# Kernel tuning notes

Hardware: AMD Instinct MI355X
Metric: run time of the kernel (lower is better)

The kernel has to match this reference:

```python
import jax, jax.numpy as jnp
import numpy as np

N_NODES = 100000
NEG_SLOPE = 0.2


def glorot(key, shape):
    fan_in, fan_out = shape[0], shape[-1]
    lim = jnp.sqrt(6.0 / (fan_in + fan_out))
    return jax.random.uniform(key, shape, jnp.float32, -lim, lim)


def setup_inputs() -> dict:
    key = jax.random.key(0)
    ks = jax.random.split(key, 16)
    x = jax.random.normal(ks[0], (N_NODES, 128), jnp.float32)
    edge_index = jax.random.randint(ks[1], (2, 1600000), 0, N_NODES, jnp.int64)
    H1, C1 = 4, 32
    C2 = 64
    return {
        "x": x,
        "edge_index": edge_index,
        # layer 1: GATv2Conv(128 -> 32, heads=4, concat)
        "Wl1": glorot(ks[2], (128, H1 * C1)), "bl1": jnp.zeros((H1 * C1,), jnp.float32),
        "Wr1": glorot(ks[3], (128, H1 * C1)), "br1": jnp.zeros((H1 * C1,), jnp.float32),
        "att1": glorot(ks[4], (H1, C1)),
        "bias1": jnp.zeros((H1 * C1,), jnp.float32),
        # layer 2: GATv2Conv(128 -> 64, heads=1, concat)
        "Wl2": glorot(ks[5], (H1 * C1, C2)), "bl2": jnp.zeros((C2,), jnp.float32),
        "Wr2": glorot(ks[6], (H1 * C1, C2)), "br2": jnp.zeros((C2,), jnp.float32),
        "att2": glorot(ks[7], (1, C2)),
        "bias2": jnp.zeros((C2,), jnp.float32),
    }


def gatv2_layer(x, src, dst, Wl, bl, Wr, br, att, bias):
    # x: [N, F_in]; src/dst: [E] (self-loops already appended)
    H, C = att.shape
    n = x.shape[0]
    xl = (x @ Wl + bl).reshape(n, H, C)  # source transform
    xr = (x @ Wr + br).reshape(n, H, C)  # target transform
    e = jax.nn.leaky_relu(xl[src] + xr[dst], NEG_SLOPE)          # [E, H, C]
    score = jnp.einsum('ehc,hc->eh', e, att)                     # [E, H]
    # segment softmax over incoming edges of each destination node
    smax = jax.ops.segment_max(score, dst, num_segments=n)       # [N, H]
    ex = jnp.exp(score - smax[dst])
    denom = jax.ops.segment_sum(ex, dst, num_segments=n)
    alpha = ex / denom[dst]                                      # [E, H]
    out = jax.ops.segment_sum(alpha[:, :, None] * xl[src], dst, num_segments=n)
    return out.reshape(n, H * C) + bias


def reference(x, edge_index, Wl1, bl1, Wr1, br1, att1, bias1,
              Wl2, bl2, Wr2, br2, att2, bias2):
    n = x.shape[0]
    loops = jnp.arange(n, dtype=edge_index.dtype)
    src = jnp.concatenate([edge_index[0], loops])
    dst = jnp.concatenate([edge_index[1], loops])
    h = gatv2_layer(x, src, dst, Wl1, bl1, Wr1, br1, att1, bias1)
    h = jax.nn.relu(h)
    out = gatv2_layer(h, src, dst, Wl2, bl2, Wr2, br2, att2, bias2)
    return out
```

## Files before the change

kernel.cpp:

```cpp
#include <hip/hip_runtime.h>
#include <hip/hip_fp16.h>

#define NEG 0.2f

typedef _Float16 f16x8 __attribute__((ext_vector_type(8)));
typedef _Float16 f16x2 __attribute__((ext_vector_type(2)));
typedef float    f32x4 __attribute__((ext_vector_type(4)));

__device__ __forceinline__ float fdot2h(__half2 a, __half2 b, float c) {
    return __builtin_amdgcn_fdot2(__builtin_bit_cast(f16x2, a),
                                  __builtin_bit_cast(f16x2, b), c, false);
}

__device__ __forceinline__ __half2 u2h2(unsigned int u) {
    return __builtin_bit_cast(__half2, u);
}

__device__ __forceinline__ __half2 hmax2(__half2 a, __half2 b) {
    unsigned int ua = __builtin_bit_cast(unsigned int, a);
    unsigned int ub = __builtin_bit_cast(unsigned int, b);
    unsigned int ud;
    asm("v_pk_max_f16 %0, %1, %2" : "=v"(ud) : "v"(ua), "v"(ub));
    return __builtin_bit_cast(__half2, ud);
}

template<int CTRL>
__device__ __forceinline__ float dppadd(float x) {
    int xi = __builtin_bit_cast(int, x);
    int yi = __builtin_amdgcn_update_dpp(0, xi, CTRL, 0xf, 0xf, true);
    return x + __builtin_bit_cast(float, yi);
}

template<int COLS, bool IN_F16, bool HPL>
__global__ __launch_bounds__(256) void xform_k(
    const float* __restrict__ Xf, const __half* __restrict__ Xh,
    const float* __restrict__ Wl, const float* __restrict__ bl,
    const float* __restrict__ Wr, const float* __restrict__ br,
    __half* __restrict__ YL, __half* __restrict__ YR, int nrows)
{
    constexpr int CPW = COLS / 2;
    __shared__ _Float16 Ws[COLS * 136];

    const int t = threadIdx.x;
    for (int i = t; i < 128 * COLS; i += 256) {
        int k = i / COLS, c = i % COLS;
        const float* Wp = (c >= CPW) ? Wr : Wl;
        int lc = c - ((c >= CPW) ? CPW : 0);
        Ws[c * 136 + k] = (_Float16)Wp[(long)k * CPW + lc];
    }
    __syncthreads();

    const int lane = t & 63, wv = t >> 6;
    const int m = lane & 15, quad = lane >> 4;

    float bv[COLS / 16];
    #pragma unroll
    for (int ct = 0; ct < COLS / 16; ++ct) {
        int col = ct * 16 + m;
        bv[ct] = (col >= CPW) ? br[col - CPW] : bl[col];
    }

    const int ntiles = (nrows + 15) >> 4;
    const int stride = gridDim.x * 4;

    int tile = blockIdx.x * 4 + wv;
    if (tile >= ntiles) return;

    f16x8 A0[4], A1[4];

    auto loadA = [&](int tl, f16x8* Af) {
        int row = tl * 16 + m;
        if (row >= nrows) row = nrows - 1;
        if constexpr (IN_F16) {
            const uint4* Xp = (const uint4*)(Xh + (long)row * 128);
            #pragma unroll
            for (int ks = 0; ks < 4; ++ks) {
                uint4 v = Xp[ks * 4 + quad];
                Af[ks] = __builtin_bit_cast(f16x8, v);
            }
        } else {
            const float4* Xp = (const float4*)(Xf + (long)row * 128);
            #pragma unroll
            for (int ks = 0; ks < 4; ++ks) {
                float4 a = Xp[ks * 8 + quad * 2];
                float4 b = Xp[ks * 8 + quad * 2 + 1];
                _Float16 h[8] = {(_Float16)a.x,(_Float16)a.y,(_Float16)a.z,(_Float16)a.w,
                                 (_Float16)b.x,(_Float16)b.y,(_Float16)b.z,(_Float16)b.w};
                Af[ks] = *(f16x8*)h;
            }
        }
    };

    loadA(tile, A0);

    for (; tile < ntiles; tile += stride) {
        int nt = tile + stride;
        if (nt < ntiles) loadA(nt, A1);

        const int row0 = tile * 16;
        #pragma unroll
        for (int ct = 0; ct < COLS / 16; ++ct) {
            f32x4 acc = (f32x4){0.f, 0.f, 0.f, 0.f};
            #pragma unroll
            for (int ks = 0; ks < 4; ++ks) {
                f16x8 Bf = *(const f16x8*)&Ws[(ct * 16 + m) * 136 + ks * 32 + quad * 8];
                acc = __builtin_amdgcn_mfma_f32_16x16x32_f16(A0[ks], Bf, acc, 0, 0, 0);
            }
            int col = ct * 16 + m;
            int which = col >= CPW;
            int lc = col - (which ? CPW : 0);
            _Float16* Y = (_Float16*)(which ? YR : YL);
            int rb = row0 + quad * 4;
            #pragma unroll
            for (int g = 0; g < 4; ++g) {
                int r = rb + g;
                if (r < nrows) {
                    long idx;
                    if (HPL && !which)
                        idx = (long)(lc >> 6) * ((long)nrows * 64) + (long)r * 64 + (lc & 63);
                    else
                        idx = (long)r * CPW + lc;
                    Y[idx] = (_Float16)(acc[g] + bv[ct]);
                }
            }
        }
        #pragma unroll
        for (int ks = 0; ks < 4; ++ks) A0[ks] = A1[ks];
    }
}

__global__ __launch_bounds__(256) void h1_k(
    const int* __restrict__ ei, int* __restrict__ gh, int E0, int ET, int NBK)
{
    __shared__ int h[256];
    const int t = threadIdx.x, blk = blockIdx.x;
    h[t] = 0;
    __syncthreads();
    int e = blk * 4096 + t;
    #pragma unroll
    for (int u = 0; u < 16; ++u, e += 256) {
        if (e < ET) {
            int dst = (e < E0) ? ei[E0 + e] : (e - E0);
            atomicAdd(&h[dst >> 9], 1);
        }
    }
    __syncthreads();
    gh[t * NBK + blk] = h[t];
}

__global__ __launch_bounds__(256) void scan1_k(
    const int* __restrict__ cnt, int* __restrict__ loc, int* __restrict__ bsum, int n)
{
    __shared__ int wsum[4];
    int t = threadIdx.x;
    int i0 = blockIdx.x * 1024 + t * 4;
    int4 v;
    v.x = (i0 + 0 < n) ? cnt[i0 + 0] : 0;
    v.y = (i0 + 1 < n) ? cnt[i0 + 1] : 0;
    v.z = (i0 + 2 < n) ? cnt[i0 + 2] : 0;
    v.w = (i0 + 3 < n) ? cnt[i0 + 3] : 0;
    int tsum = v.x + v.y + v.z + v.w;
    int incl = tsum;
    #pragma unroll
    for (int s = 1; s < 64; s <<= 1) {
        int u = __shfl_up(incl, s, 64);
        if ((t & 63) >= s) incl += u;
    }
    int wid = t >> 6;
    if ((t & 63) == 63) wsum[wid] = incl;
    __syncthreads();
    int woff = 0;
    #pragma unroll
    for (int w = 0; w < 4; ++w) if (w < wid) woff += wsum[w];
    int ex = woff + incl - tsum;
    if (i0 + 0 < n) loc[i0 + 0] = ex;
    if (i0 + 1 < n) loc[i0 + 1] = ex + v.x;
    if (i0 + 2 < n) loc[i0 + 2] = ex + v.x + v.y;
    if (i0 + 3 < n) loc[i0 + 3] = ex + v.x + v.y + v.z;
    if (t == 255) bsum[blockIdx.x] = woff + incl;
}

__global__ void scan2_k(const int* __restrict__ bsum, int* __restrict__ bcarry,
                        int M, int* __restrict__ total_out)
{
    int lane = threadIdx.x;
    int carry = 0;
    for (int base = 0; base < M; base += 64) {
        int i = base + lane;
        int v = (i < M) ? bsum[i] : 0;
        int incl = v;
        #pragma unroll
        for (int s = 1; s < 64; s <<= 1) {
            int u = __shfl_up(incl, s, 64);
            if (lane >= s) incl += u;
        }
        if (i < M) bcarry[i] = carry + incl - v;
        carry += __shfl(incl, 63, 64);
    }
    if (lane == 0) *total_out = carry;
}

__global__ __launch_bounds__(256) void scan3_k(
    int* __restrict__ off, const int* __restrict__ bcarry, int n)
{
    int i = blockIdx.x * 256 + threadIdx.x;
    if (i >= n) return;
    off[i] += bcarry[i >> 10];
}

__global__ __launch_bounds__(256) void sc1_k(
    const int* __restrict__ ei, const int* __restrict__ gh,
    uint2* __restrict__ rec, int E0, int ET, int NBK)
{
    __shared__ int lofs[256];
    const int t = threadIdx.x, blk = blockIdx.x;
    lofs[t] = gh[t * NBK + blk];
    __syncthreads();
    int e = blk * 4096 + t;
    #pragma unroll
    for (int u = 0; u < 16; ++u, e += 256) {
        if (e < ET) {
            int src = (e < E0) ? ei[e]      : (e - E0);
            int dst = (e < E0) ? ei[E0 + e] : (e - E0);
            int p = atomicAdd(&lofs[dst >> 9], 1);
            rec[p] = make_uint2((unsigned)src, (unsigned)dst);
        }
    }
}

__global__ __launch_bounds__(256) void p2_k(
    const uint2* __restrict__ rec, const int* __restrict__ gh,
    int* __restrict__ srcs, int* __restrict__ off, int N, int NBK)
{
    __shared__ int hist[512];
    __shared__ int sc[2][512];
    __shared__ int curo[512];
    const int t = threadIdx.x;
    const int b = blockIdx.x;
    const int base = gh[b * NBK];
    const int end  = gh[(b + 1) * NBK];
    hist[t] = 0; hist[t + 256] = 0;
    __syncthreads();
    for (int i = base + t; i < end; i += 256) {
        uint2 r = rec[i];
        atomicAdd(&hist[r.y & 511], 1);
    }
    __syncthreads();
    sc[0][t] = hist[t]; sc[0][t + 256] = hist[t + 256];
    __syncthreads();
    int pp = 0;
    for (int s = 1; s < 512; s <<= 1, pp ^= 1) {
        int j0 = t, j1 = t + 256;
        sc[pp ^ 1][j0] = sc[pp][j0] + ((j0 >= s) ? sc[pp][j0 - s] : 0);
        sc[pp ^ 1][j1] = sc[pp][j1] + ((j1 >= s) ? sc[pp][j1 - s] : 0);
        __syncthreads();
    }
    {
        int j0 = t, j1 = t + 256;
        int e0 = base + sc[pp][j0] - hist[j0];
        int e1 = base + sc[pp][j1] - hist[j1];
        curo[j0] = e0;
        curo[j1] = e1;
        int d0 = b * 512 + j0, d1 = b * 512 + j1;
        if (d0 < N) off[d0] = e0;
        if (d1 < N) off[d1] = e1;
    }
    __syncthreads();
    for (int i = base + t; i < end; i += 256) {
        uint2 r = rec[i];
        int pos = atomicAdd(&curo[r.y & 511], 1);
        srcs[pos] = (int)r.x;
    }
}

template<bool RELU>
__global__ __launch_bounds__(256) void fused128hp_k(
    const __half* __restrict__ XLp, const __half* __restrict__ XR,
    const float* __restrict__ ATT, const int* __restrict__ srcs,
    const int* __restrict__ off, const float* __restrict__ bias,
    __half* __restrict__ OUT, int N, int p)
{
    const int t   = threadIdx.x;
    const int d   = blockIdx.x * 32 + (t >> 3);
    const int sub = t & 7;
    const bool nv = d < N;

    int a = 0, b = 0;
    if (nv) { a = off[d]; b = off[d + 1]; }

    __half2 xr[4] = { u2h2(0), u2h2(0), u2h2(0), u2h2(0) };
    if (nv) {
        uint4 ur = *(const uint4*)(XR + (long)d * 128 + p * 64 + sub * 8);
        xr[0] = u2h2(ur.x); xr[1] = u2h2(ur.y); xr[2] = u2h2(ur.z); xr[3] = u2h2(ur.w);
    }
    float4 at0f = ((const float4*)ATT)[p * 16 + sub * 2];
    float4 at1f = ((const float4*)ATT)[p * 16 + sub * 2 + 1];
    __half2 at[4] = { __floats2half2_rn(at0f.x, at0f.y), __floats2half2_rn(at0f.z, at0f.w),
                      __floats2half2_rn(at1f.x, at1f.y), __floats2half2_rn(at1f.z, at1f.w) };
    const __half2 neg2 = __float2half2_rn(NEG);

    float l = 0.f;
    float accv[8] = {0.f,0.f,0.f,0.f,0.f,0.f,0.f,0.f};

    const uint4* XL4 = (const uint4*)(XLp + (size_t)p * N * 64);

    if (b > a) {
        const int bm1 = b - 1;
        int sA = srcs[a];
        uint4 r0 = XL4[(long)sA * 8 + sub];
        int i1 = (a + 1 < bm1) ? a + 1 : bm1;
        int sB = srcs[i1];
        uint4 r1 = XL4[(long)sB * 8 + sub];
        int i2 = (a + 2 < bm1) ? a + 2 : bm1;
        int s2 = srcs[i2];

        for (int e = a; e < b; ++e) {
            uint4 r2 = XL4[(long)s2 * 8 + sub];
            int i3 = (e + 3 < bm1) ? e + 3 : bm1;
            int s3 = srcs[i3];

            __half2 x0 = u2h2(r0.x), x1 = u2h2(r0.y), x2 = u2h2(r0.z), x3 = u2h2(r0.w);
            __half2 s0h = __hadd2(x0, xr[0]);
            __half2 s1h = __hadd2(x1, xr[1]);
            __half2 s2h = __hadd2(x2, xr[2]);
            __half2 s3h = __hadd2(x3, xr[3]);
            __half2 q0 = hmax2(s0h, __hmul2(s0h, neg2));
            __half2 q1 = hmax2(s1h, __hmul2(s1h, neg2));
            __half2 q2 = hmax2(s2h, __hmul2(s2h, neg2));
            __half2 q3 = hmax2(s3h, __hmul2(s3h, neg2));
            float p0 = fdot2h(q0, at[0], 0.f);
            p0 = fdot2h(q1, at[1], p0);
            p0 = fdot2h(q2, at[2], p0);
            p0 = fdot2h(q3, at[3], p0);
            p0 = dppadd<0xB1>(p0);
            p0 = dppadd<0x4E>(p0);
            float ex = __expf(p0);
            l += ex;
            float2 f0 = __half22float2(x0), f1 = __half22float2(x1);
            float2 f2 = __half22float2(x2), f3 = __half22float2(x3);
            accv[0] += ex * f0.x; accv[1] += ex * f0.y;
            accv[2] += ex * f1.x; accv[3] += ex * f1.y;
            accv[4] += ex * f2.x; accv[5] += ex * f2.y;
            accv[6] += ex * f3.x; accv[7] += ex * f3.y;

            r0 = r1; r1 = r2; s2 = s3;
        }
    }

    if (nv) {
        float inv = 1.f / l;
        float4 b0 = ((const float4*)bias)[p * 16 + sub * 2];
        float4 b1 = ((const float4*)bias)[p * 16 + sub * 2 + 1];
        float o[8] = { accv[0]*inv + b0.x, accv[1]*inv + b0.y,
                       accv[2]*inv + b0.z, accv[3]*inv + b0.w,
                       accv[4]*inv + b1.x, accv[5]*inv + b1.y,
                       accv[6]*inv + b1.z, accv[7]*inv + b1.w };
        if constexpr (RELU) {
            #pragma unroll
            for (int j = 0; j < 8; ++j) o[j] = fmaxf(o[j], 0.f);
        }
        uint4 uo;
        uo.x = __builtin_bit_cast(unsigned int, __floats2half2_rn(o[0], o[1]));
        uo.y = __builtin_bit_cast(unsigned int, __floats2half2_rn(o[2], o[3]));
        uo.z = __builtin_bit_cast(unsigned int, __floats2half2_rn(o[4], o[5]));
        uo.w = __builtin_bit_cast(unsigned int, __floats2half2_rn(o[6], o[7]));
        *(uint4*)(OUT + (long)d * 128 + p * 64 + sub * 8) = uo;
    }
}

template<bool RELU>
__global__ __launch_bounds__(256) void fused64_k(
    const __half* __restrict__ XL, const __half* __restrict__ XR,
    const float* __restrict__ ATT, const int* __restrict__ srcs,
    const int* __restrict__ off, const float* __restrict__ bias,
    float* __restrict__ OUT, int N)
{
    const int t   = threadIdx.x;
    const int d   = blockIdx.x * 32 + (t >> 3);
    const int sub = t & 7;
    const bool nv = d < N;

    int a = 0, b = 0;
    if (nv) { a = off[d]; b = off[d + 1]; }

    __half2 xr[4] = { u2h2(0), u2h2(0), u2h2(0), u2h2(0) };
    if (nv) {
        uint4 ur = *(const uint4*)(XR + (long)d * 64 + sub * 8);
        xr[0] = u2h2(ur.x); xr[1] = u2h2(ur.y); xr[2] = u2h2(ur.z); xr[3] = u2h2(ur.w);
    }
    float4 at0f = ((const float4*)ATT)[sub * 2];
    float4 at1f = ((const float4*)ATT)[sub * 2 + 1];
    __half2 at[4] = { __floats2half2_rn(at0f.x, at0f.y), __floats2half2_rn(at0f.z, at0f.w),
                      __floats2half2_rn(at1f.x, at1f.y), __floats2half2_rn(at1f.z, at1f.w) };
    const __half2 neg2 = __float2half2_rn(NEG);

    float l = 0.f;
    float accv[8] = {0.f,0.f,0.f,0.f,0.f,0.f,0.f,0.f};

    const uint4* XL4 = (const uint4*)XL;

    if (b > a) {
        const int bm1 = b - 1;
        int sA = srcs[a];
        uint4 r0 = XL4[(long)sA * 8 + sub];
        int i1 = (a + 1 < bm1) ? a + 1 : bm1;
        int sB = srcs[i1];
        uint4 r1 = XL4[(long)sB * 8 + sub];
        int i2 = (a + 2 < bm1) ? a + 2 : bm1;
        int s2 = srcs[i2];

        for (int e = a; e < b; ++e) {
            uint4 r2 = XL4[(long)s2 * 8 + sub];
            int i3 = (e + 3 < bm1) ? e + 3 : bm1;
            int s3 = srcs[i3];

            __half2 x0 = u2h2(r0.x), x1 = u2h2(r0.y), x2 = u2h2(r0.z), x3 = u2h2(r0.w);
            __half2 s0h = __hadd2(x0, xr[0]);
            __half2 s1h = __hadd2(x1, xr[1]);
            __half2 s2h = __hadd2(x2, xr[2]);
            __half2 s3h = __hadd2(x3, xr[3]);
            __half2 q0 = hmax2(s0h, __hmul2(s0h, neg2));
            __half2 q1 = hmax2(s1h, __hmul2(s1h, neg2));
            __half2 q2 = hmax2(s2h, __hmul2(s2h, neg2));
            __half2 q3 = hmax2(s3h, __hmul2(s3h, neg2));
            float p0 = fdot2h(q0, at[0], 0.f);
            p0 = fdot2h(q1, at[1], p0);
            p0 = fdot2h(q2, at[2], p0);
            p0 = fdot2h(q3, at[3], p0);
            p0 = dppadd<0xB1>(p0);
            p0 = dppadd<0x4E>(p0);
            p0 = dppadd<0x141>(p0);
            float ex = __expf(p0);
            l += ex;
            float2 f0 = __half22float2(x0), f1 = __half22float2(x1);
            float2 f2 = __half22float2(x2), f3 = __half22float2(x3);
            accv[0] += ex * f0.x; accv[1] += ex * f0.y;
            accv[2] += ex * f1.x; accv[3] += ex * f1.y;
            accv[4] += ex * f2.x; accv[5] += ex * f2.y;
            accv[6] += ex * f3.x; accv[7] += ex * f3.y;

            r0 = r1; r1 = r2; s2 = s3;
        }
    }

    if (nv) {
        float inv = 1.f / l;
        float4 b0 = ((const float4*)bias)[sub * 2];
        float4 b1 = ((const float4*)bias)[sub * 2 + 1];
        float4 o0 = make_float4(accv[0]*inv + b0.x, accv[1]*inv + b0.y,
                                accv[2]*inv + b0.z, accv[3]*inv + b0.w);
        float4 o1 = make_float4(accv[4]*inv + b1.x, accv[5]*inv + b1.y,
                                accv[6]*inv + b1.z, accv[7]*inv + b1.w);
        if constexpr (RELU) {
            o0.x = fmaxf(o0.x, 0.f); o0.y = fmaxf(o0.y, 0.f);
            o0.z = fmaxf(o0.z, 0.f); o0.w = fmaxf(o0.w, 0.f);
            o1.x = fmaxf(o1.x, 0.f); o1.y = fmaxf(o1.y, 0.f);
            o1.z = fmaxf(o1.z, 0.f); o1.w = fmaxf(o1.w, 0.f);
        }
        *(float4*)(OUT + (long)d * 64 + sub * 8)     = o0;
        *(float4*)(OUT + (long)d * 64 + sub * 8 + 4) = o1;
    }
}

extern "C" void kernel_launch(void* const* d_in, const int* in_sizes, int n_in,
                              void* d_out, int out_size, void* d_ws, size_t ws_size,
                              hipStream_t stream)
{
    const float* x     = (const float*)d_in[0];
    const int*   ei    = (const int*)  d_in[1];
    const float* Wl1   = (const float*)d_in[2];
    const float* bl1   = (const float*)d_in[3];
    const float* Wr1   = (const float*)d_in[4];
    const float* br1   = (const float*)d_in[5];
    const float* att1  = (const float*)d_in[6];
    const float* bias1 = (const float*)d_in[7];
    const float* Wl2   = (const float*)d_in[8];
    const float* bl2   = (const float*)d_in[9];
    const float* Wr2   = (const float*)d_in[10];
    const float* br2   = (const float*)d_in[11];
    const float* att2  = (const float*)d_in[12];
    const float* bias2 = (const float*)d_in[13];

    const int  N  = in_sizes[0] / 128;
    const int  E0 = in_sizes[1] / 2;
    const int  ET = E0 + N;

    char* w = (char*)d_ws;
    __half* XLh = (__half*)w;
    __half* XRh = XLh + (size_t)N * 128;
    __half* Cch = XRh + (size_t)N * 128;
    int*    off = (int*)(Cch + (size_t)N * 128);
    int*    srcs= off + (N + 1);
    int*    gh  = srcs + ET;
    uint2*  rec = (uint2*)w;
    float*  out = (float*)d_out;

    dim3 b256(256);
    const int ng32  = (N + 31) / 32;

    const int NBK   = (ET + 4095) / 4096;
    const int n1    = 256 * NBK;
    const int NB1   = (n1 + 1023) / 1024;
    const int NBUCK = (N + 511) / 512;
    int* bsum = gh + n1;
    int* bcar = bsum + NB1;

    h1_k<<<NBK, b256, 0, stream>>>(ei, gh, E0, ET, NBK);
    scan1_k<<<NB1, b256, 0, stream>>>(gh, gh, bsum, n1);
    scan2_k<<<1, 64, 0, stream>>>(bsum, bcar, NB1, off + N);
    scan3_k<<<(n1 + 255) / 256, b256, 0, stream>>>(gh, bcar, n1);
    sc1_k<<<NBK, b256, 0, stream>>>(ei, gh, rec, E0, ET, NBK);
    p2_k<<<NBUCK, b256, 0, stream>>>(rec, gh, srcs, off, N, NBK);

    xform_k<256, false, true><<<512, b256, 0, stream>>>(
        x, nullptr, Wl1, bl1, Wr1, br1, XLh, XRh, N);
    fused128hp_k<true><<<ng32, b256, 0, stream>>>(XLh, XRh, att1, srcs, off, bias1, Cch, N, 0);
    fused128hp_k<true><<<ng32, b256, 0, stream>>>(XLh, XRh, att1, srcs, off, bias1, Cch, N, 1);

    xform_k<128, true, false><<<1024, b256, 0, stream>>>(
        nullptr, Cch, Wl2, bl2, Wr2, br2, XLh, XRh, N);
    fused64_k<false><<<ng32, b256, 0, stream>>>(XLh, XRh, att2, srcs, off, bias2, out, N);
}
```

Baseline: 367.9 us.

## Merge layer-1 transform with dst histogram and batch both head-pair launches

Folds the destination-histogram pass into the layer-1 feature transform kernel, so extra blocks beyond the transform blocks count edges while the others run MFMA GEMMs. The edge-record scratch buffer moves from the start of the workspace to the Cch region, because XLh/XRh are now written before the sort and must not be overwritten. The two per-head-pair aggregation launches become one launch with a 2D grid. This removes launches and lets the GEMM overlap the edge-counting work. The cost is a heavier shared-memory footprint for the histogram blocks, which reduces how many of them fit on a CU.

```diff
diff --git a/kernel.cpp b/kernel.cpp
--- a/kernel.cpp
+++ b/kernel.cpp
@@ -29,6 +29,114 @@
     int xi = __builtin_bit_cast(int, x);
     int yi = __builtin_amdgcn_update_dpp(0, xi, CTRL, 0xf, 0xf, true);
     return x + __builtin_bit_cast(float, yi);
+}
+
+__global__ __launch_bounds__(256) void xf1_h1_k(
+    const float* __restrict__ Xf,
+    const float* __restrict__ Wl, const float* __restrict__ bl,
+    const float* __restrict__ Wr, const float* __restrict__ br,
+    __half* __restrict__ YL, __half* __restrict__ YR, int nrows,
+    const int* __restrict__ ei, int* __restrict__ gh, int E0, int ET, int NBK,
+    int XBLKS)
+{
+    __shared__ _Float16 Ws[256 * 136];
+    const int t = threadIdx.x;
+
+    if ((int)blockIdx.x >= XBLKS) {
+        int* h = (int*)Ws;
+        const int hb = blockIdx.x - XBLKS;
+        h[t] = 0;
+        __syncthreads();
+        int e = hb * 4096 + t;
+        #pragma unroll
+        for (int u = 0; u < 16; ++u, e += 256) {
+            if (e < ET) {
+                int dst = (e < E0) ? ei[E0 + e] : (e - E0);
+                atomicAdd(&h[dst >> 9], 1);
+            }
+        }
+        __syncthreads();
+        gh[t * NBK + hb] = h[t];
+        return;
+    }
+
+    constexpr int COLS = 256, CPW = 128;
+    for (int i = t; i < 128 * COLS; i += 256) {
+        int k = i / COLS, c = i % COLS;
+        const float* Wp = (c >= CPW) ? Wr : Wl;
+        int lc = c - ((c >= CPW) ? CPW : 0);
+        Ws[c * 136 + k] = (_Float16)Wp[(long)k * CPW + lc];
+    }
+    __syncthreads();
+
+    const int lane = t & 63, wv = t >> 6;
+    const int m = lane & 15, quad = lane >> 4;
+
+    float bv[COLS / 16];
+    #pragma unroll
+    for (int ct = 0; ct < COLS / 16; ++ct) {
+        int col = ct * 16 + m;
+        bv[ct] = (col >= CPW) ? br[col - CPW] : bl[col];
+    }
+
+    const int ntiles = (nrows + 15) >> 4;
+    const int stride = XBLKS * 4;
+
+    int tile = blockIdx.x * 4 + wv;
+    if (tile >= ntiles) return;
+
+    f16x8 A0[4], A1[4];
+
+    auto loadA = [&](int tl, f16x8* Af) {
+        int row = tl * 16 + m;
+        if (row >= nrows) row = nrows - 1;
+        const float4* Xp = (const float4*)(Xf + (long)row * 128);
+        #pragma unroll
+        for (int ks = 0; ks < 4; ++ks) {
+            float4 a = Xp[ks * 8 + quad * 2];
+            float4 b = Xp[ks * 8 + quad * 2 + 1];
+            _Float16 h8[8] = {(_Float16)a.x,(_Float16)a.y,(_Float16)a.z,(_Float16)a.w,
+                              (_Float16)b.x,(_Float16)b.y,(_Float16)b.z,(_Float16)b.w};
+            Af[ks] = *(f16x8*)h8;
+        }
+    };
+
+    loadA(tile, A0);
+
+    for (; tile < ntiles; tile += stride) {
+        int nt = tile + stride;
+        if (nt < ntiles) loadA(nt, A1);
+
+        const int row0 = tile * 16;
+        #pragma unroll
+        for (int ct = 0; ct < COLS / 16; ++ct) {
+            f32x4 acc = (f32x4){0.f, 0.f, 0.f, 0.f};
+            #pragma unroll
+            for (int ks = 0; ks < 4; ++ks) {
+                f16x8 Bf = *(const f16x8*)&Ws[(ct * 16 + m) * 136 + ks * 32 + quad * 8];
+                acc = __builtin_amdgcn_mfma_f32_16x16x32_f16(A0[ks], Bf, acc, 0, 0, 0);
+            }
+            int col = ct * 16 + m;
+            int which = col >= CPW;
+            int lc = col - (which ? CPW : 0);
+            _Float16* Y = (_Float16*)(which ? YR : YL);
+            int rb = row0 + quad * 4;
+            #pragma unroll
+            for (int g = 0; g < 4; ++g) {
+                int r = rb + g;
+                if (r < nrows) {
+                    long idx;
+                    if (!which)
+                        idx = (long)(lc >> 6) * ((long)nrows * 64) + (long)r * 64 + (lc & 63);
+                    else
+                        idx = (long)r * CPW + lc;
+                    Y[idx] = (_Float16)(acc[g] + bv[ct]);
+                }
+            }
+        }
+        #pragma unroll
+        for (int ks = 0; ks < 4; ++ks) A0[ks] = A1[ks];
+    }
 }
 
 template<int COLS, bool IN_F16, bool HPL>
@@ -84,9 +192,9 @@
             for (int ks = 0; ks < 4; ++ks) {
                 float4 a = Xp[ks * 8 + quad * 2];
                 float4 b = Xp[ks * 8 + quad * 2 + 1];
-                _Float16 h[8] = {(_Float16)a.x,(_Float16)a.y,(_Float16)a.z,(_Float16)a.w,
-                                 (_Float16)b.x,(_Float16)b.y,(_Float16)b.z,(_Float16)b.w};
-                Af[ks] = *(f16x8*)h;
+                _Float16 h8[8] = {(_Float16)a.x,(_Float16)a.y,(_Float16)a.z,(_Float16)a.w,
+                                  (_Float16)b.x,(_Float16)b.y,(_Float16)b.z,(_Float16)b.w};
+                Af[ks] = *(f16x8*)h8;
             }
         }
     };
@@ -129,25 +237,6 @@
     }
 }
 
-__global__ __launch_bounds__(256) void h1_k(
-    const int* __restrict__ ei, int* __restrict__ gh, int E0, int ET, int NBK)
-{
-    __shared__ int h[256];
-    const int t = threadIdx.x, blk = blockIdx.x;
-    h[t] = 0;
-    __syncthreads();
-    int e = blk * 4096 + t;
-    #pragma unroll
-    for (int u = 0; u < 16; ++u, e += 256) {
-        if (e < ET) {
-            int dst = (e < E0) ? ei[E0 + e] : (e - E0);
-            atomicAdd(&h[dst >> 9], 1);
-        }
-    }
-    __syncthreads();
-    gh[t * NBK + blk] = h[t];
-}
-
 __global__ __launch_bounds__(256) void scan1_k(
     const int* __restrict__ cnt, int* __restrict__ loc, int* __restrict__ bsum, int n)
 {
@@ -278,9 +367,10 @@
     const __half* __restrict__ XLp, const __half* __restrict__ XR,
     const float* __restrict__ ATT, const int* __restrict__ srcs,
     const int* __restrict__ off, const float* __restrict__ bias,
-    __half* __restrict__ OUT, int N, int p)
+    __half* __restrict__ OUT, int N)
 {
     const int t   = threadIdx.x;
+    const int p   = blockIdx.y;
     const int d   = blockIdx.x * 32 + (t >> 3);
     const int sub = t & 7;
     const bool nv = d < N;
@@ -492,7 +582,7 @@
     int*    off = (int*)(Cch + (size_t)N * 128);
     int*    srcs= off + (N + 1);
     int*    gh  = srcs + ET;
-    uint2*  rec = (uint2*)w;
+    uint2*  rec = (uint2*)Cch;
     float*  out = (float*)d_out;
 
     dim3 b256(256);
@@ -505,17 +595,19 @@
     int* bsum = gh + n1;
     int* bcar = bsum + NB1;
 
-    h1_k<<<NBK, b256, 0, stream>>>(ei, gh, E0, ET, NBK);
+    const int XBLKS = 512;
+
+    xf1_h1_k<<<XBLKS + NBK, b256, 0, stream>>>(
+        x, Wl1, bl1, Wr1, br1, XLh, XRh, N, ei, gh, E0, ET, NBK, XBLKS);
+
     scan1_k<<<NB1, b256, 0, stream>>>(gh, gh, bsum, n1);
     scan2_k<<<1, 64, 0, stream>>>(bsum, bcar, NB1, off + N);
     scan3_k<<<(n1 + 255) / 256, b256, 0, stream>>>(gh, bcar, n1);
     sc1_k<<<NBK, b256, 0, stream>>>(ei, gh, rec, E0, ET, NBK);
     p2_k<<<NBUCK, b256, 0, stream>>>(rec, gh, srcs, off, N, NBK);
 
-    xform_k<256, false, true><<<512, b256, 0, stream>>>(
-        x, nullptr, Wl1, bl1, Wr1, br1, XLh, XRh, N);
-    fused128hp_k<true><<<ng32, b256, 0, stream>>>(XLh, XRh, att1, srcs, off, bias1, Cch, N, 0);
-    fused128hp_k<true><<<ng32, b256, 0, stream>>>(XLh, XRh, att1, srcs, off, bias1, Cch, N, 1);
+    fused128hp_k<true><<<dim3(ng32, 2), b256, 0, stream>>>(
+        XLh, XRh, att1, srcs, off, bias1, Cch, N);
 
     xform_k<128, true, false><<<1024, b256, 0, stream>>>(
         nullptr, Cch, Wl2, bl2, Wr2, br2, XLh, XRh, N);
```

Measured after the change: 372.0 us (median of 2 runs). About the same (+1.1%).

## Pre-transpose weights once and fuse edge histogram into layer-1 transform launch

Applied to the files above, without the earlier changes.

A small kernel now converts the weights to transposed fp16 a single time, so the transform kernels read B fragments straight from global memory instead of staging them in LDS in every block. The dst-bucket histogram runs as extra blocks in the layer-1 transform launch, and the two per-half attention launches become one 2D grid. The record buffer moves into the Cch region so it no longer overlaps the XL/XR outputs that are now written before the sort. The risk is that global B-fragment reads with a 256-byte row stride may be less efficient than the LDS path.

```diff
diff --git a/kernel.cpp b/kernel.cpp
--- a/kernel.cpp
+++ b/kernel.cpp
@@ -31,24 +31,50 @@
     return x + __builtin_bit_cast(float, yi);
 }
 
-template<int COLS, bool IN_F16, bool HPL>
-__global__ __launch_bounds__(256) void xform_k(
+__global__ __launch_bounds__(256) void wt_k(
+    const float* __restrict__ Wl1, const float* __restrict__ Wr1,
+    const float* __restrict__ Wl2, const float* __restrict__ Wr2,
+    _Float16* __restrict__ W1t, _Float16* __restrict__ W2t)
+{
+    const int b = blockIdx.x, t = threadIdx.x;
+    const float* src = (b == 0) ? Wl1 : (b == 1) ? Wr1 : (b == 2) ? Wl2 : Wr2;
+    const int CP = (b < 2) ? 128 : 64;
+    _Float16* dst = (b < 2) ? (W1t + (b == 1 ? 128 * 128 : 0))
+                            : (W2t + (b == 3 ? 64 * 128 : 0));
+    for (int i = t; i < 128 * CP; i += 256) {
+        int k = i / CP, c = i % CP;
+        dst[c * 128 + k] = (_Float16)src[i];
+    }
+}
+
+template<int COLS, int CPW, bool IN_F16, bool HPL, bool DO_H1>
+__global__ __launch_bounds__(256) void xform2_k(
     const float* __restrict__ Xf, const __half* __restrict__ Xh,
-    const float* __restrict__ Wl, const float* __restrict__ bl,
-    const float* __restrict__ Wr, const float* __restrict__ br,
-    __half* __restrict__ YL, __half* __restrict__ YR, int nrows)
-{
-    constexpr int CPW = COLS / 2;
-    __shared__ _Float16 Ws[COLS * 136];
-
+    const _Float16* __restrict__ Wt,
+    const float* __restrict__ bl, const float* __restrict__ br,
+    __half* __restrict__ YL, __half* __restrict__ YR, int nrows,
+    const int* __restrict__ ei, int* __restrict__ gh,
+    int E0, int ET, int NBK, int XBLKS)
+{
     const int t = threadIdx.x;
-    for (int i = t; i < 128 * COLS; i += 256) {
-        int k = i / COLS, c = i % COLS;
-        const float* Wp = (c >= CPW) ? Wr : Wl;
-        int lc = c - ((c >= CPW) ? CPW : 0);
-        Ws[c * 136 + k] = (_Float16)Wp[(long)k * CPW + lc];
-    }
-    __syncthreads();
+
+    if (DO_H1 && (int)blockIdx.x >= XBLKS) {
+        __shared__ int h[256];
+        const int hb = blockIdx.x - XBLKS;
+        h[t] = 0;
+        __syncthreads();
+        int e = hb * 4096 + t;
+        #pragma unroll
+        for (int u = 0; u < 16; ++u, e += 256) {
+            if (e < ET) {
+                int dst = (e < E0) ? ei[E0 + e] : (e - E0);
+                atomicAdd(&h[dst >> 9], 1);
+            }
+        }
+        __syncthreads();
+        gh[t * NBK + hb] = h[t];
+        return;
+    }
 
     const int lane = t & 63, wv = t >> 6;
     const int m = lane & 15, quad = lane >> 4;
@@ -61,7 +87,7 @@
     }
 
     const int ntiles = (nrows + 15) >> 4;
-    const int stride = gridDim.x * 4;
+    const int stride = XBLKS * 4;
 
     int tile = blockIdx.x * 4 + wv;
     if (tile >= ntiles) return;
@@ -84,9 +110,9 @@
             for (int ks = 0; ks < 4; ++ks) {
                 float4 a = Xp[ks * 8 + quad * 2];
                 float4 b = Xp[ks * 8 + quad * 2 + 1];
-                _Float16 h[8] = {(_Float16)a.x,(_Float16)a.y,(_Float16)a.z,(_Float16)a.w,
-                                 (_Float16)b.x,(_Float16)b.y,(_Float16)b.z,(_Float16)b.w};
-                Af[ks] = *(f16x8*)h;
+                _Float16 h8[8] = {(_Float16)a.x,(_Float16)a.y,(_Float16)a.z,(_Float16)a.w,
+                                  (_Float16)b.x,(_Float16)b.y,(_Float16)b.z,(_Float16)b.w};
+                Af[ks] = *(f16x8*)h8;
             }
         }
     };
@@ -103,7 +129,7 @@
             f32x4 acc = (f32x4){0.f, 0.f, 0.f, 0.f};
             #pragma unroll
             for (int ks = 0; ks < 4; ++ks) {
-                f16x8 Bf = *(const f16x8*)&Ws[(ct * 16 + m) * 136 + ks * 32 + quad * 8];
+                f16x8 Bf = *(const f16x8*)&Wt[(ct * 16 + m) * 128 + ks * 32 + quad * 8];
                 acc = __builtin_amdgcn_mfma_f32_16x16x32_f16(A0[ks], Bf, acc, 0, 0, 0);
             }
             int col = ct * 16 + m;
@@ -129,25 +155,6 @@
     }
 }
 
-__global__ __launch_bounds__(256) void h1_k(
-    const int* __restrict__ ei, int* __restrict__ gh, int E0, int ET, int NBK)
-{
-    __shared__ int h[256];
-    const int t = threadIdx.x, blk = blockIdx.x;
-    h[t] = 0;
-    __syncthreads();
-    int e = blk * 4096 + t;
-    #pragma unroll
-    for (int u = 0; u < 16; ++u, e += 256) {
-        if (e < ET) {
-            int dst = (e < E0) ? ei[E0 + e] : (e - E0);
-            atomicAdd(&h[dst >> 9], 1);
-        }
-    }
-    __syncthreads();
-    gh[t * NBK + blk] = h[t];
-}
-
 __global__ __launch_bounds__(256) void scan1_k(
     const int* __restrict__ cnt, int* __restrict__ loc, int* __restrict__ bsum, int n)
 {
@@ -278,9 +285,10 @@
     const __half* __restrict__ XLp, const __half* __restrict__ XR,
     const float* __restrict__ ATT, const int* __restrict__ srcs,
     const int* __restrict__ off, const float* __restrict__ bias,
-    __half* __restrict__ OUT, int N, int p)
+    __half* __restrict__ OUT, int N)
 {
     const int t   = threadIdx.x;
+    const int p   = blockIdx.y;
     const int d   = blockIdx.x * 32 + (t >> 3);
     const int sub = t & 7;
     const bool nv = d < N;
@@ -492,7 +500,7 @@
     int*    off = (int*)(Cch + (size_t)N * 128);
     int*    srcs= off + (N + 1);
     int*    gh  = srcs + ET;
-    uint2*  rec = (uint2*)w;
+    uint2*  rec = (uint2*)Cch;
     float*  out = (float*)d_out;
 
     dim3 b256(256);
@@ -504,20 +512,26 @@
     const int NBUCK = (N + 511) / 512;
     int* bsum = gh + n1;
     int* bcar = bsum + NB1;
-
-    h1_k<<<NBK, b256, 0, stream>>>(ei, gh, E0, ET, NBK);
+    _Float16* W1t = (_Float16*)(bcar + NB1);
+    _Float16* W2t = W1t + 256 * 128;
+
+    const int XBLKS = 1024;
+
+    wt_k<<<4, b256, 0, stream>>>(Wl1, Wr1, Wl2, Wr2, W1t, W2t);
+
+    xform2_k<256, 128, false, true, true><<<XBLKS + NBK, b256, 0, stream>>>(
+        x, nullptr, W1t, bl1, br1, XLh, XRh, N, ei, gh, E0, ET, NBK, XBLKS);
+
     scan1_k<<<NB1, b256, 0, stream>>>(gh, gh, bsum, n1);
     scan2_k<<<1, 64, 0, stream>>>(bsum, bcar, NB1, off + N);
     scan3_k<<<(n1 + 255) / 256, b256, 0, stream>>>(gh, bcar, n1);
     sc1_k<<<NBK, b256, 0, stream>>>(ei, gh, rec, E0, ET, NBK);
     p2_k<<<NBUCK, b256, 0, stream>>>(rec, gh, srcs, off, N, NBK);
 
-    xform_k<256, false, true><<<512, b256, 0, stream>>>(
-        x, nullptr, Wl1, bl1, Wr1, br1, XLh, XRh, N);
-    fused128hp_k<true><<<ng32, b256, 0, stream>>>(XLh, XRh, att1, srcs, off, bias1, Cch, N, 0);
-    fused128hp_k<true><<<ng32, b256, 0, stream>>>(XLh, XRh, att1, srcs, off, bias1, Cch, N, 1);
-
-    xform_k<128, true, false><<<1024, b256, 0, stream>>>(
-        nullptr, Cch, Wl2, bl2, Wr2, br2, XLh, XRh, N);
+    fused128hp_k<true><<<dim3(ng32, 2), b256, 0, stream>>>(
+        XLh, XRh, att1, srcs, off, bias1, Cch, N);
+
+    xform2_k<128, 64, true, false, false><<<1024, b256, 0, stream>>>(
+        nullptr, Cch, W2t, bl2, br2, XLh, XRh, N, nullptr, nullptr, 0, 0, 0, 1024);
     fused64_k<false><<<ng32, b256, 0, stream>>>(XLh, XRh, att2, srcs, off, bias2, out, N);
 }
```

After: 407.4 us. +10.7%, slower.
